# Optimization experiments

Hardware: AMD Instinct MI355X
Metric: run time of the kernel (lower is better)

The kernel has to match this reference:

```python
import jax, jax.numpy as jnp
import numpy as np

M = 7
EPS = 1e-8

def setup_inputs() -> dict:
    key = jax.random.key(0)
    ks = jax.random.split(key, 6)
    B, C, H, W = 8, 256, 128, 128
    return {
        "x": jax.random.normal(ks[0], (B, C, H, W), dtype=jnp.float32),
        "w1": jax.random.normal(ks[1], (M * M, 32), dtype=jnp.float32) * 0.1,
        "b1": jnp.zeros((32,), dtype=jnp.float32),
        "w2": jax.random.normal(ks[2], (32, 3), dtype=jnp.float32) * 0.1,
        "b2": jnp.zeros((3,), dtype=jnp.float32),
        "wr": jax.random.normal(ks[3], (256, 256), dtype=jnp.float32) * (1.0 / 16.0),
    }

def _aniso_kernels(params):
    # params: [B,3] -> normalized anisotropic Gaussian kernels [B,M,M]
    theta = jnp.arctan2(params[:, 0], params[:, 1]) / 2.0 + jnp.pi / 2.0
    lam1 = jnp.exp(params[:, 2])
    lam2 = 1.0 / (lam1 + EPS)
    lin = jnp.linspace(-(M // 2), M // 2, M, dtype=params.dtype)
    yy, xx = jnp.meshgrid(lin, lin, indexing="ij")  # matches torch.meshgrid 'ij'
    cos_t = jnp.cos(theta)[:, None, None]
    sin_t = jnp.sin(theta)[:, None, None]
    x_rot = xx * cos_t + yy * sin_t
    y_rot = -xx * sin_t + yy * cos_t
    k = jnp.exp(-(x_rot ** 2 / (2.0 * lam1[:, None, None] ** 2)
                  + y_rot ** 2 / (2.0 * lam2[:, None, None] ** 2)))
    return k / (k.sum(axis=(1, 2), keepdims=True) + EPS)

def reference(x, w1, b1, w2, b2, wr):
    B, C, H, W = x.shape
    xf = jnp.fft.fftshift(jnp.fft.fft2(x, norm="ortho"), axes=(-2, -1))
    # center m x m crop of channel-mean magnitude
    mag = jnp.abs(xf).mean(axis=1)  # [B,H,W]
    h0, w0 = H // 2 - M // 2, W // 2 - M // 2
    center = mag[:, h0:h0 + M, w0:w0 + M].reshape(B, M * M)
    hid = jax.nn.relu(center @ w1 + b1)
    params = hid @ w2 + b2  # [B,3]
    kern = _aniso_kernels(params)  # [B,M,M], shared across channels per sample
    # depthwise filtering: one 7x7 kernel per sample applied to all 2C (real|imag) channels
    stacked = jnp.concatenate([xf.real, xf.imag], axis=1)  # [B,2C,H,W]
    pad = [(M // 2, M // 2)] * 2
    def conv_one(img, k):  # img [2C,H,W], k [M,M]
        return jax.lax.conv_general_dilated(img[:, None], k[None, None],
                                            (1, 1), pad)[:, 0]
    filt = jax.vmap(conv_one)(stacked, kern)  # [B,2C,H,W]
    real_f, imag_f = filt[:, :C], filt[:, C:]
    rr = jnp.einsum("bchw,oc->bohw", real_f, wr)  # refine_conv 1x1, no bias
    ii = jnp.einsum("bchw,oc->bohw", imag_f, wr)
    out_f = jnp.fft.ifftshift(jax.lax.complex(rr, ii), axes=(-2, -1))
    return jnp.fft.ifft2(out_f, norm="ortho").real + x
```

## Files before the change

kernel.cpp:

```cpp
#include <hip/hip_runtime.h>

#define HW 16384
#define PIf 3.14159265358979323846f
typedef unsigned short ushortt;
typedef unsigned int uint32;
typedef __attribute__((ext_vector_type(8))) short short8;
typedef __attribute__((ext_vector_type(4))) float f32x4;
typedef __attribute__((ext_vector_type(2))) float f32x2;
typedef __attribute__((ext_vector_type(2))) unsigned int uintv2;

__device__ __forceinline__ float bf2f(ushortt b) {
    return __uint_as_float(((unsigned)b) << 16);
}
__device__ __forceinline__ ushortt f2bf(float f) {
    unsigned u = __float_as_uint(f);
    u += 0x7fffu + ((u >> 16) & 1u);
    return (ushortt)(u >> 16);
}
__device__ __forceinline__ int brev6(int v) { return (int)(__brev((unsigned)v) >> 26); }

__device__ __forceinline__ void bfly(float& Ar, float& Ai, float& Br, float& Bi,
                                     float tr, float ti) {
    float sr = Ar + Br, si = Ai + Bi;
    float dr = Ar - Br, di = Ai - Bi;
    Ar = sr; Ai = si;
    Br = dr * tr - di * ti;
    Bi = dr * ti + di * tr;
}

__device__ __forceinline__ void xswap32(float& a, float& b) {
    uintv2 r = __builtin_amdgcn_permlane32_swap(__float_as_uint(a), __float_as_uint(b), false, false);
    a = __uint_as_float(r.x); b = __uint_as_float(r.y);
}
__device__ __forceinline__ void xswap16(float& a, float& b) {
    uintv2 r = __builtin_amdgcn_permlane16_swap(__float_as_uint(a), __float_as_uint(b), false, false);
    a = __uint_as_float(r.x); b = __uint_as_float(r.y);
}
template<int IMM>
__device__ __forceinline__ void pswap_sw(float& a, float& b, bool up) {
    float sel = up ? a : b;
    float rcv = __int_as_float(__builtin_amdgcn_ds_swizzle(__float_as_int(sel), IMM));
    a = up ? rcv : a;
    b = up ? b : rcv;
}
template<int CTRL>
__device__ __forceinline__ void pswap_dpp(float& a, float& b, bool up) {
    float sel = up ? a : b;
    float rcv = __int_as_float(__builtin_amdgcn_update_dpp(0, __float_as_int(sel), CTRL, 0xF, 0xF, true));
    a = up ? rcv : a;
    b = up ? b : rcv;
}

struct TwSet { float r0,i0,r1,i1,r2,i2,r3,i3,r4,i4,r5,i5; };

__device__ __forceinline__ TwSet load_tw(const float* __restrict__ twr,
                                         const float* __restrict__ twi, int l) {
    TwSet t;
    t.r0 = twr[l];            t.i0 = twi[l];
    t.r1 = twr[(l & 31) << 1]; t.i1 = twi[(l & 31) << 1];
    t.r2 = twr[(l & 15) << 2]; t.i2 = twi[(l & 15) << 2];
    t.r3 = twr[(l & 7)  << 3]; t.i3 = twi[(l & 7)  << 3];
    t.r4 = twr[(l & 3)  << 4]; t.i4 = twi[(l & 3)  << 4];
    t.r5 = twr[(l & 1)  << 5]; t.i5 = twi[(l & 1)  << 5];
    return t;
}

__device__ __forceinline__ void fft128_ps(float& Ar, float& Ai, float& Br, float& Bi,
                                          const TwSet& t,
                                          bool u8, bool u4, bool u2, bool u1) {
    bfly(Ar, Ai, Br, Bi, t.r0, t.i0);
    xswap32(Ar, Br); xswap32(Ai, Bi);
    bfly(Ar, Ai, Br, Bi, t.r1, t.i1);
    xswap16(Ar, Br); xswap16(Ai, Bi);
    bfly(Ar, Ai, Br, Bi, t.r2, t.i2);
    pswap_sw<0x201F>(Ar, Br, u8); pswap_sw<0x201F>(Ai, Bi, u8);
    bfly(Ar, Ai, Br, Bi, t.r3, t.i3);
    pswap_sw<0x101F>(Ar, Br, u4); pswap_sw<0x101F>(Ai, Bi, u4);
    bfly(Ar, Ai, Br, Bi, t.r4, t.i4);
    pswap_dpp<0x4E>(Ar, Br, u2); pswap_dpp<0x4E>(Ai, Bi, u2);
    bfly(Ar, Ai, Br, Bi, t.r5, t.i5);
    pswap_dpp<0xB1>(Ar, Br, u1); pswap_dpp<0xB1>(Ai, Bi, u1);
    {
        float sr = Ar + Br, si = Ai + Bi;
        float dr = Ar - Br, di = Ai - Bi;
        Ar = sr; Ai = si; Br = dr; Bi = di;
    }
}

__global__ __launch_bounds__(1024) void fft_fwd(const float* __restrict__ x,
                                                ushortt* __restrict__ xfRe,
                                                ushortt* __restrict__ xfIm,
                                                float* __restrict__ magc) {
    __shared__ float2 sc[128][129];
    __shared__ float twr[64], twi[64];
    int img = blockIdx.x;
    int tid = threadIdx.x, l = tid & 63, wv = tid >> 6;
    if (tid < 64) {
        float s, c;
        sincosf(-PIf * (float)tid / 64.0f, &s, &c);
        twr[tid] = c; twi[tid] = s;
    }
    const float* xi = x + (size_t)img * HW;
    __syncthreads();

    TwSet t = load_tw(twr, twi, l);
    bool u8 = (l & 8) != 0, u4 = (l & 4) != 0, u2 = (l & 2) != 0, u1 = (l & 1) != 0;
    int e = brev6(l);

    float lar[4], lai[4], lbr[4], lbi[4];
    #pragma unroll
    for (int r = 0; r < 4; ++r) {
        int p = wv * 4 + r;
        lar[r] = xi[(2 * p) * 128 + l];
        lai[r] = xi[(2 * p + 1) * 128 + l];
        lbr[r] = xi[(2 * p) * 128 + 64 + l];
        lbi[r] = xi[(2 * p + 1) * 128 + 64 + l];
    }
    #pragma unroll
    for (int r = 0; r < 4; ++r) {
        int p = wv * 4 + r;
        float Ar = lar[r], Ai = lai[r], Br = lbr[r], Bi = lbi[r];
        fft128_ps(Ar, Ai, Br, Bi, t, u8, u4, u2, u1);
        sc[p][e]      = make_float2(Ar, Ai);
        sc[p][e + 64] = make_float2(Br, Bi);
    }
    __syncthreads();

    float oar[8], oai[8], obr[8], obi[8];
    int pa = l >> 1, pb = 32 + (l >> 1);
    bool odd = (l & 1) != 0;
    #pragma unroll
    for (int r = 0; r < 8; ++r) {
        int c = wv * 8 + r, cm = (128 - c) & 127;
        float2 Za = sc[pa][c], Zma = sc[pa][cm];
        float2 Zb = sc[pb][c], Zmb = sc[pb][cm];
        float Ar = odd ? (Za.y + Zma.y) : (Za.x + Zma.x);
        float Ai = odd ? (Zma.x - Za.x) : (Za.y - Zma.y);
        float Br = odd ? (Zb.y + Zmb.y) : (Zb.x + Zmb.x);
        float Bi = odd ? (Zmb.x - Zb.x) : (Zb.y - Zmb.y);
        fft128_ps(Ar, Ai, Br, Bi, t, u8, u4, u2, u1);
        oar[r] = Ar; oai[r] = Ai; obr[r] = Br; obi[r] = Bi;
    }
    __syncthreads();
    #pragma unroll
    for (int r = 0; r < 8; ++r) {
        int c = wv * 8 + r;
        sc[e][c]      = make_float2(oar[r], oai[r]);
        sc[e + 64][c] = make_float2(obr[r], obi[r]);
    }
    __syncthreads();

    uint32* oRe = (uint32*)(xfRe + ((size_t)img << 14));
    uint32* oIm = (uint32*)(xfIm + ((size_t)img << 14));
    for (int idx2 = tid; idx2 < 8192; idx2 += 1024) {
        int p = idx2 >> 6, qp = idx2 & 63, q = qp * 2;
        int u  = (p + 64) & 127;
        int v0 = (q + 64) & 127;
        const float scl = 1.0f / 256.0f;
        float2 e0 = sc[u][v0], e1 = sc[u][v0 + 1];
        uint32 re = (uint32)f2bf(e0.x * scl) | ((uint32)f2bf(e1.x * scl) << 16);
        uint32 im = (uint32)f2bf(e0.y * scl) | ((uint32)f2bf(e1.y * scl) << 16);
        oRe[p * 64 + qp] = re;
        oIm[p * 64 + qp] = im;
    }
    if (tid < 49) {
        int p = 61 + tid / 7, q = 61 + tid % 7;
        int u = (p + 64) & 127, v = (q + 64) & 127;
        float2 z = sc[u][v];
        float mag = sqrtf(z.x * z.x + z.y * z.y) * (1.0f / 256.0f);
        atomicAdd(&magc[(img >> 8) * 49 + tid], mag);
    }
}

__global__ __launch_bounds__(256) void mlp_kern(const float* __restrict__ magc,
                                                const float* __restrict__ w1,
                                                const float* __restrict__ b1,
                                                const float* __restrict__ w2,
                                                const float* __restrict__ b2,
                                                float2* __restrict__ kern_pk) {
    __shared__ float hid[8][32];
    __shared__ float par[8][3];
    __shared__ float kun[8][49];
    __shared__ float ksum[8];
    int tid = threadIdx.x;
    {
        int b = tid >> 5, n = tid & 31;
        float acc = b1[n];
        for (int i = 0; i < 49; ++i)
            acc = fmaf(magc[b * 49 + i] * (1.0f / 256.0f), w1[i * 32 + n], acc);
        hid[b][n] = fmaxf(acc, 0.f);
    }
    __syncthreads();
    if (tid < 24) {
        int b = tid / 3, j = tid % 3;
        float acc = b2[j];
        for (int n = 0; n < 32; ++n) acc = fmaf(hid[b][n], w2[n * 3 + j], acc);
        par[b][j] = acc;
    }
    __syncthreads();
    for (int idx = tid; idx < 392; idx += 256) {
        int b = idx / 49, ij = idx % 49;
        int i = ij / 7, j2 = ij % 7;
        float p0 = par[b][0], p1 = par[b][1], p2 = par[b][2];
        float theta = atan2f(p0, p1) * 0.5f + PIf * 0.5f;
        float lam1 = expf(p2);
        float lam2 = 1.0f / (lam1 + 1e-8f);
        float yy = (float)(i - 3), xx = (float)(j2 - 3);
        float ct, st;
        sincosf(theta, &st, &ct);
        float xr =  xx * ct + yy * st;
        float yr = -xx * st + yy * ct;
        kun[b][ij] = expf(-(xr * xr / (2.f * lam1 * lam1) + yr * yr / (2.f * lam2 * lam2)));
    }
    __syncthreads();
    if (tid < 8) {
        float s = 0.f;
        for (int t = 0; t < 49; ++t) s += kun[tid][t];
        ksum[tid] = s + 1e-8f;
    }
    __syncthreads();
    for (int idx = tid; idx < 448; idx += 256) {
        int b  = idx / 56;
        int r7 = idx - b * 56;
        int rr = r7 / 7, dx = r7 - rr * 7;
        float inv = 1.0f / ksum[b];
        float v0 = (rr < 7)  ? kun[b][rr * 7 + dx] * inv       : 0.f;
        float v1 = (rr >= 1) ? kun[b][(rr - 1) * 7 + dx] * inv : 0.f;
        kern_pk[idx] = make_float2(v0, v1);
    }
}

__global__ __launch_bounds__(256) void gemm_mix(const ushortt* __restrict__ xfRe,
                                                const ushortt* __restrict__ xfIm,
                                                const float* __restrict__ wr,
                                                ushortt* __restrict__ mixRe,
                                                ushortt* __restrict__ mixIm) {
    __shared__ ushortt lA[2][5120];
    __shared__ uint32  lB[2][2560];
    int tid = threadIdx.x;
    int lane = tid & 63, wave = tid >> 6;
    int wm = wave >> 1, wn = wave & 1;
    int l15 = lane & 15, q4 = lane >> 4;
    int b = blockIdx.z >> 1, part = blockIdx.z & 1;
    const ushortt* Xb = (part ? xfIm : xfRe) + (size_t)b * (256 * HW)
                        + blockIdx.x * 128;
    ushortt* Dst = (part ? mixIm : mixRe) + (size_t)b * (256 * HW)
                   + (size_t)(blockIdx.y * 128) * HW + blockIdx.x * 128;
    const float* W = wr + (blockIdx.y * 128) * 256;

    int srow = tid >> 1, shalf = tid & 1;
    const float* wRow = W + srow * 256 + shalf * 16;
    int ldsOffA = srow * 40 + shalf * 16;

    int kt = tid >> 4;
    int pq = tid & 15;
    int kswz = kt ^ ((pq & 3) << 2);
    int rowbase = pq * 160;

    float4 wreg[4];
    uint4  a0, a1;
    #pragma unroll
    for (int i = 0; i < 4; ++i) wreg[i] = *(const float4*)(wRow + i * 4);
    {
        const ushortt* xp = Xb + (size_t)(2 * kt) * HW + pq * 8;
        a0 = *(const uint4*)xp;
        a1 = *(const uint4*)(xp + HW);
    }

    f32x4 acc[4][4];
    #pragma unroll
    for (int i = 0; i < 4; ++i)
        #pragma unroll
        for (int j = 0; j < 4; ++j)
            #pragma unroll
            for (int k = 0; k < 4; ++k) acc[i][j][k] = 0.f;

    int abase = (wm * 64 + l15) * 40 + q4 * 8;
    int baddr[4];
    #pragma unroll
    for (int f = 0; f < 4; ++f) {
        int pf = wn * 64 + f * 16 + l15;
        baddr[f] = pf * 40 + ((q4 ^ ((pf >> 3) & 3)) << 3);
    }

    for (int kb = 0; kb < 8; ++kb) {
        int bufc = kb & 1;
        {
            float ff[16] = {wreg[0].x, wreg[0].y, wreg[0].z, wreg[0].w,
                            wreg[1].x, wreg[1].y, wreg[1].z, wreg[1].w,
                            wreg[2].x, wreg[2].y, wreg[2].z, wreg[2].w,
                            wreg[3].x, wreg[3].y, wreg[3].z, wreg[3].w};
            uint32 p[8];
            #pragma unroll
            for (int j = 0; j < 8; ++j)
                p[j] = (uint32)f2bf(ff[2 * j]) | ((uint32)f2bf(ff[2 * j + 1]) << 16);
            *(uint4*)&lA[bufc][ldsOffA]     = make_uint4(p[0], p[1], p[2], p[3]);
            *(uint4*)&lA[bufc][ldsOffA + 8] = make_uint4(p[4], p[5], p[6], p[7]);
        }
        {
            uint32 d[8];
            d[0] = (a0.x & 0xffffu) | (a1.x << 16);
            d[1] = (a0.x >> 16)     | (a1.x & 0xffff0000u);
            d[2] = (a0.y & 0xffffu) | (a1.y << 16);
            d[3] = (a0.y >> 16)     | (a1.y & 0xffff0000u);
            d[4] = (a0.z & 0xffffu) | (a1.z << 16);
            d[5] = (a0.z >> 16)     | (a1.z & 0xffff0000u);
            d[6] = (a0.w & 0xffffu) | (a1.w << 16);
            d[7] = (a0.w >> 16)     | (a1.w & 0xffff0000u);
            uint32* lb = lB[bufc];
            #pragma unroll
            for (int j = 0; j < 8; ++j) lb[rowbase + j * 20 + kswz] = d[j];
        }
        __syncthreads();
        if (kb < 7) {
            const float* wN = wRow + (kb + 1) * 32;
            #pragma unroll
            for (int i = 0; i < 4; ++i) wreg[i] = *(const float4*)(wN + i * 4);
            const ushortt* xp = Xb + (size_t)((kb + 1) * 32 + 2 * kt) * HW + pq * 8;
            a0 = *(const uint4*)xp;
            a1 = *(const uint4*)(xp + HW);
        }
        short8 af[4], bf[4];
        const ushortt* lbU = (const ushortt*)lB[bufc];
        #pragma unroll
        for (int f = 0; f < 4; ++f) af[f] = *(const short8*)&lA[bufc][abase + f * 640];
        #pragma unroll
        for (int f = 0; f < 4; ++f) bf[f] = *(const short8*)&lbU[baddr[f]];
        #pragma unroll
        for (int fi = 0; fi < 4; ++fi)
            #pragma unroll
            for (int fj = 0; fj < 4; ++fj)
                acc[fi][fj] = __builtin_amdgcn_mfma_f32_16x16x32_bf16(
                    af[fi], bf[fj], acc[fi][fj], 0, 0, 0);
    }
    #pragma unroll
    for (int fi = 0; fi < 4; ++fi) {
        #pragma unroll
        for (int r = 0; r < 4; ++r) {
            int o_l = wm * 64 + fi * 16 + q4 * 4 + r;
            ushortt* dp = Dst + (size_t)o_l * HW + wn * 64 + l15;
            #pragma unroll
            for (int fj = 0; fj < 4; ++fj)
                dp[fj * 16] = f2bf(acc[fi][fj][r]);
        }
    }
}

__global__ __launch_bounds__(256) void conv7(const ushortt* __restrict__ mixRe,
                                             const ushortt* __restrict__ mixIm,
                                             const float2* __restrict__ kern_pk,
                                             ushortt* __restrict__ outRe,
                                             ushortt* __restrict__ outIm) {
    __shared__ float tile[70 * 73];
    int b = blockIdx.z;
    int plane = blockIdx.y;
    int part = plane >> 8;
    size_t pbase = ((size_t)(b * 256 + (plane & 255))) << 14;
    const ushortt* src = (part ? mixIm : mixRe) + pbase;
    ushortt* dst = (part ? outIm : outRe) + pbase;
    int ty = (blockIdx.x >> 1) * 64, tx = (blockIdx.x & 1) * 64;
    int tid = threadIdx.x;
    const float2* kp = kern_pk + b * 56;

    for (int idx = tid; idx < 2520; idx += 256) {
        int row = idx / 36, du = idx - row * 36;
        int gy = ty + row - 3, gx0 = tx - 4 + 2 * du;
        uint32 v = 0u;
        if ((unsigned)gy < 128u && (unsigned)gx0 < 128u)
            v = *(const uint32*)(src + gy * 128 + gx0);
        int base = row * 73 + 2 * du;
        tile[base]     = __uint_as_float(v << 16);
        tile[base + 1] = __uint_as_float(v & 0xffff0000u);
    }
    __syncthreads();

    int ox = (tid & 7) * 8, oy = (tid >> 3) * 2;
    f32x2 acc2[8];
    #pragma unroll
    for (int j = 0; j < 8; ++j) { acc2[j].x = 0.f; acc2[j].y = 0.f; }

    #pragma unroll
    for (int dyy = 0; dyy < 8; ++dyy) {
        float row[14];
        #pragma unroll
        for (int m = 0; m < 14; ++m) row[m] = tile[(oy + dyy) * 73 + ox + 1 + m];
        #pragma unroll
        for (int dx = 0; dx < 7; ++dx) {
            float2 kl = kp[dyy * 7 + dx];
            f32x2 kk; kk.x = kl.x; kk.y = kl.y;
            #pragma unroll
            for (int j = 0; j < 8; ++j) {
                f32x2 rr; rr.x = row[dx + j]; rr.y = row[dx + j];
                acc2[j] = __builtin_elementwise_fma(rr, kk, acc2[j]);
            }
        }
    }

    uint32 s0[4], s1[4];
    #pragma unroll
    for (int m = 0; m < 4; ++m) {
        s0[m] = (uint32)f2bf(acc2[2 * m].x) | ((uint32)f2bf(acc2[2 * m + 1].x) << 16);
        s1[m] = (uint32)f2bf(acc2[2 * m].y) | ((uint32)f2bf(acc2[2 * m + 1].y) << 16);
    }
    *(uint4*)(dst + (ty + oy) * 128 + tx + ox)     = make_uint4(s0[0], s0[1], s0[2], s0[3]);
    *(uint4*)(dst + (ty + oy + 1) * 128 + tx + ox) = make_uint4(s1[0], s1[1], s1[2], s1[3]);
}

__global__ __launch_bounds__(1024) void ifft_add(const ushortt* __restrict__ convRe,
                                                 const ushortt* __restrict__ convIm,
                                                 const float* __restrict__ x,
                                                 float* __restrict__ out) {
    __shared__ float2 sc[128][129];
    __shared__ float twr[64], twi[64];
    int img = blockIdx.x;
    int tid = threadIdx.x, l = tid & 63, wv = tid >> 6;
    if (tid < 64) {
        float s, c;
        sincosf(-PIf * (float)tid / 64.0f, &s, &c);
        twr[tid] = c; twi[tid] = s;
    }
    const ushortt* cr = convRe + ((size_t)img << 14);
    const ushortt* ci = convIm + ((size_t)img << 14);
    __syncthreads();

    TwSet t = load_tw(twr, twi, l);
    bool u8 = (l & 8) != 0, u4 = (l & 4) != 0, u2 = (l & 2) != 0, u1 = (l & 1) != 0;
    int e = brev6(l);

    {
        float nar[8], nai[8], nbr[8], nbi[8];
        #pragma unroll
        for (int r = 0; r < 8; ++r) {
            int p = ((wv * 8 + r) + 64) & 127;
            nar[r] = bf2f(cr[p * 128 + 64 + l]);
            nai[r] = bf2f(ci[p * 128 + 64 + l]);
            nbr[r] = bf2f(cr[p * 128 + l]);
            nbi[r] = bf2f(ci[p * 128 + l]);
        }
        #pragma unroll
        for (int r = 0; r < 8; ++r) {
            int u = wv * 8 + r;
            float Ar = nar[r], Ai = -nai[r], Br = nbr[r], Bi = -nbi[r];
            fft128_ps(Ar, Ai, Br, Bi, t, u8, u4, u2, u1);
            sc[u][e]      = make_float2(Ar, Ai);
            sc[u][e + 64] = make_float2(Br, Bi);
        }
    }
    __syncthreads();

    float oar[4], oai[4], obr[4], obi[4];
    int rv  = (128 - l) & 127;
    int rv2 = (64 - l) & 127;
    #pragma unroll
    for (int r = 0; r < 4; ++r) {
        int m = wv * 4 + r;
        int c0 = 2 * m, c1 = 2 * m + 1;
        float2 P  = sc[l][c0],      R  = sc[l][c1];
        float2 Q  = sc[rv][c0],     S  = sc[rv][c1];
        float2 P2 = sc[l + 64][c0], R2 = sc[l + 64][c1];
        float2 Q2 = sc[rv2][c0],    S2 = sc[rv2][c1];
        float Ar = P.x + Q.x - R.y + S.y;
        float Ai = P.y - Q.y + R.x + S.x;
        float Br = P2.x + Q2.x - R2.y + S2.y;
        float Bi = P2.y - Q2.y + R2.x + S2.x;
        fft128_ps(Ar, Ai, Br, Bi, t, u8, u4, u2, u1);
        oar[r] = Ar; oai[r] = Ai; obr[r] = Br; obi[r] = Bi;
    }
    __syncthreads();
    #pragma unroll
    for (int r = 0; r < 4; ++r) {
        int m = wv * 4 + r;
        sc[e][m]      = make_float2(oar[r], oai[r]);
        sc[e + 64][m] = make_float2(obr[r], obi[r]);
    }
    __syncthreads();

    const float* xi = x + (size_t)img * HW;
    float* oo = out + (size_t)img * HW;
    for (int idx2 = tid; idx2 < 8192; idx2 += 1024) {
        int y = idx2 >> 6, m = idx2 & 63;
        float2 v = sc[y][m];
        float2 xv = *(const float2*)(xi + y * 128 + 2 * m);
        float2 ov;
        ov.x = v.x * (1.0f / 256.0f) + xv.x;
        ov.y = v.y * (1.0f / 256.0f) + xv.y;
        *(float2*)(oo + y * 128 + 2 * m) = ov;
    }
}

extern "C" void kernel_launch(void* const* d_in, const int* in_sizes, int n_in,
                              void* d_out, int out_size, void* d_ws, size_t ws_size,
                              hipStream_t stream) {
    const float* x  = (const float*)d_in[0];
    const float* w1 = (const float*)d_in[1];
    const float* b1 = (const float*)d_in[2];
    const float* w2 = (const float*)d_in[3];
    const float* b2 = (const float*)d_in[4];
    const float* wr = (const float*)d_in[5];

    char* ws = (char*)d_ws;
    ushortt* xfRe  = (ushortt*)ws;
    ushortt* xfIm  = xfRe + 33554432;
    ushortt* mixRe = (ushortt*)(ws + 134217728);
    ushortt* mixIm = mixRe + 33554432;
    ushortt* convRe = xfRe, *convIm = xfIm;
    float* magc = (float*)(ws + 268435456);
    float2* kern_pk = (float2*)(ws + 268435456 + 2048);

    hipMemsetAsync(magc, 0, 392 * sizeof(float), stream);
    fft_fwd<<<2048, 1024, 0, stream>>>(x, xfRe, xfIm, magc);
    mlp_kern<<<1, 256, 0, stream>>>(magc, w1, b1, w2, b2, kern_pk);
    gemm_mix<<<dim3(128, 2, 16), 256, 0, stream>>>(xfRe, xfIm, wr, mixRe, mixIm);
    conv7<<<dim3(4, 512, 8), 256, 0, stream>>>(mixRe, mixIm, kern_pk, convRe, convIm);
    ifft_add<<<2048, 1024, 0, stream>>>(convRe, convIm, x, (float*)d_out);
}
```

Baseline: 562.2 us.

## Pack bf16 results before LDS transpose to halve fft_fwd shared memory

Column-pass FFT outputs are scaled and packed to bf16 pairs in registers, then written to a half-size LDS buffer (64x129 float2 instead of 128x129), and the final store loop just copies packed words. The center 7x7 magnitude atomics move into the column loop for the edge waves. Smaller LDS plus launch_bounds(1024,8) aims to let more blocks share a CU and to cut LDS traffic. The cost is extra register pressure and branching in the compute loop.

```diff
diff --git a/kernel.cpp b/kernel.cpp
--- a/kernel.cpp
+++ b/kernel.cpp
@@ -87,11 +87,11 @@
     }
 }
 
-__global__ __launch_bounds__(1024) void fft_fwd(const float* __restrict__ x,
-                                                ushortt* __restrict__ xfRe,
-                                                ushortt* __restrict__ xfIm,
-                                                float* __restrict__ magc) {
-    __shared__ float2 sc[128][129];
+__global__ __launch_bounds__(1024, 8) void fft_fwd(const float* __restrict__ x,
+                                                   ushortt* __restrict__ xfRe,
+                                                   ushortt* __restrict__ xfIm,
+                                                   float* __restrict__ magc) {
+    __shared__ float2 sc[64][129];
     __shared__ float twr[64], twi[64];
     int img = blockIdx.x;
     int tid = threadIdx.x, l = tid & 63, wv = tid >> 6;
@@ -126,9 +126,11 @@
     }
     __syncthreads();
 
-    float oar[8], oai[8], obr[8], obi[8];
+    uint32 pkA[8], pkB[8];
     int pa = l >> 1, pb = 32 + (l >> 1);
     bool odd = (l & 1) != 0;
+    const float scl = 1.0f / 256.0f;
+    float pAr = 0.f, pAi = 0.f, pBr = 0.f, pBi = 0.f;
     #pragma unroll
     for (int r = 0; r < 8; ++r) {
         int c = wv * 8 + r, cm = (128 - c) & 127;
@@ -139,36 +141,50 @@
         float Br = odd ? (Zb.y + Zmb.y) : (Zb.x + Zmb.x);
         float Bi = odd ? (Zmb.x - Zb.x) : (Zb.y - Zmb.y);
         fft128_ps(Ar, Ai, Br, Bi, t, u8, u4, u2, u1);
-        oar[r] = Ar; oai[r] = Ai; obr[r] = Br; obi[r] = Bi;
-    }
-    __syncthreads();
-    #pragma unroll
-    for (int r = 0; r < 8; ++r) {
-        int c = wv * 8 + r;
-        sc[e][c]      = make_float2(oar[r], oai[r]);
-        sc[e + 64][c] = make_float2(obr[r], obi[r]);
+        if (wv == 0 || wv == 15) {
+            int j7 = (c + 3) & 127;
+            if (j7 < 7) {
+                int i7a = (e + 3) & 127;
+                if (i7a < 7)
+                    atomicAdd(&magc[(img >> 8) * 49 + i7a * 7 + j7],
+                              sqrtf(Ar * Ar + Ai * Ai) * scl);
+                int i7b = (e + 67) & 127;
+                if (i7b < 7)
+                    atomicAdd(&magc[(img >> 8) * 49 + i7b * 7 + j7],
+                              sqrtf(Br * Br + Bi * Bi) * scl);
+            }
+        }
+        if (r & 1) {
+            int m = r >> 1;
+            pkA[2 * m]     = (uint32)f2bf(pAr * scl) | ((uint32)f2bf(Ar * scl) << 16);
+            pkA[2 * m + 1] = (uint32)f2bf(pAi * scl) | ((uint32)f2bf(Ai * scl) << 16);
+            pkB[2 * m]     = (uint32)f2bf(pBr * scl) | ((uint32)f2bf(Br * scl) << 16);
+            pkB[2 * m + 1] = (uint32)f2bf(pBi * scl) | ((uint32)f2bf(Bi * scl) << 16);
+        } else {
+            pAr = Ar; pAi = Ai; pBr = Br; pBi = Bi;
+        }
+    }
+    __syncthreads();
+
+    uint32* U = (uint32*)sc;
+    int m0 = wv * 4;
+    int rowoffA = (e >> 1) * 258 + 2 * (e & 1);
+    #pragma unroll
+    for (int m = 0; m < 4; ++m) {
+        *(uint2*)&U[rowoffA + 4 * (m0 + m)]        = make_uint2(pkA[2 * m], pkA[2 * m + 1]);
+        *(uint2*)&U[rowoffA + 32 * 258 + 4 * (m0 + m)] = make_uint2(pkB[2 * m], pkB[2 * m + 1]);
     }
     __syncthreads();
 
     uint32* oRe = (uint32*)(xfRe + ((size_t)img << 14));
     uint32* oIm = (uint32*)(xfIm + ((size_t)img << 14));
     for (int idx2 = tid; idx2 < 8192; idx2 += 1024) {
-        int p = idx2 >> 6, qp = idx2 & 63, q = qp * 2;
-        int u  = (p + 64) & 127;
-        int v0 = (q + 64) & 127;
-        const float scl = 1.0f / 256.0f;
-        float2 e0 = sc[u][v0], e1 = sc[u][v0 + 1];
-        uint32 re = (uint32)f2bf(e0.x * scl) | ((uint32)f2bf(e1.x * scl) << 16);
-        uint32 im = (uint32)f2bf(e0.y * scl) | ((uint32)f2bf(e1.y * scl) << 16);
-        oRe[p * 64 + qp] = re;
-        oIm[p * 64 + qp] = im;
-    }
-    if (tid < 49) {
-        int p = 61 + tid / 7, q = 61 + tid % 7;
-        int u = (p + 64) & 127, v = (q + 64) & 127;
-        float2 z = sc[u][v];
-        float mag = sqrtf(z.x * z.x + z.y * z.y) * (1.0f / 256.0f);
-        atomicAdd(&magc[(img >> 8) * 49 + tid], mag);
+        int p = idx2 >> 6, qp = idx2 & 63;
+        int u = (p + 64) & 127;
+        int m = (qp + 32) & 63;
+        uint2 v = *(const uint2*)&U[(u >> 1) * 258 + 4 * m + 2 * (u & 1)];
+        oRe[p * 64 + qp] = v.x;
+        oIm[p * 64 + qp] = v.y;
     }
 }
 
```

Result: slower. 666.4 us (+18.5%).
